# Performance work log

Measured on AMD Instinct MI355X. Metric: run time of the kernel, lower is better.

## Reference

```python
import jax, jax.numpy as jnp
import numpy as np

B, T, E, H = 64, 512, 300, 512


def lstm_scan(x, lens, W, b):
    # x: [B,T,D]; fused LSTM (LSTMBlockFusedCell semantics, forget_bias=1.0,
    # gate order i, j, f, o; outputs zeroed and state held past sequence_length).
    Bx, Tx, _ = x.shape
    Hx = b.shape[0] // 4
    xt = jnp.transpose(x, (1, 0, 2))  # [T,B,D]

    def step(carry, inp):
        c, h = carry
        x_t, t = inp
        z = jnp.concatenate([x_t, h], axis=-1) @ W + b  # [B,4H]
        i, j, f, o = jnp.split(z, 4, axis=-1)
        c_new = jax.nn.sigmoid(f + 1.0) * c + jax.nn.sigmoid(i) * jnp.tanh(j)
        h_new = jax.nn.sigmoid(o) * jnp.tanh(c_new)
        valid = (t < lens)[:, None]
        c2 = jnp.where(valid, c_new, c)
        h2 = jnp.where(valid, h_new, h)
        out = jnp.where(valid, h_new, jnp.zeros_like(h_new))
        return (c2, h2), out

    init = (jnp.zeros((Bx, Hx), x.dtype), jnp.zeros((Bx, Hx), x.dtype))
    _, ys = jax.lax.scan(step, init, (xt, jnp.arange(Tx)))
    return jnp.transpose(ys, (1, 0, 2))  # [B,T,H]


def reverse_seq(x, lens):
    # tf.reverse_sequence along time: reverse first lens[b] steps, keep padding in place
    Tx = x.shape[1]
    t = jnp.arange(Tx)[None, :]
    L = lens[:, None]
    idx = jnp.where(t < L, L - 1 - t, t)  # [B,T]
    return jnp.take_along_axis(x, idx[:, :, None], axis=1)


def bilstm(x, lens, Wf, bf, Wb, bb):
    fw = lstm_scan(x, lens, Wf, bf)
    bw = reverse_seq(lstm_scan(reverse_seq(x, lens), lens, Wb, bb), lens)
    return jnp.concatenate([fw, bw], axis=-1)  # [B,T,2H]


def setup_inputs() -> dict:
    key = jax.random.key(0)
    ks = jax.random.split(key, 8)
    s0 = 1.0 / np.sqrt(E + H)
    s1 = 1.0 / np.sqrt(2 * H + H)
    return {
        "embeddings": jax.random.normal(ks[0], (B, T, E), jnp.float32),
        "nwords": jax.random.randint(ks[1], (B,), 1, T + 1).astype(jnp.int32),
        "W_fw0": jax.random.normal(ks[2], (E + H, 4 * H), jnp.float32) * s0,
        "b_fw0": jnp.zeros((4 * H,), jnp.float32),
        "W_bw0": jax.random.normal(ks[3], (E + H, 4 * H), jnp.float32) * s0,
        "b_bw0": jnp.zeros((4 * H,), jnp.float32),
        "W_fw1": jax.random.normal(ks[4], (2 * H + H, 4 * H), jnp.float32) * s1,
        "b_fw1": jnp.zeros((4 * H,), jnp.float32),
        "W_bw1": jax.random.normal(ks[5], (2 * H + H, 4 * H), jnp.float32) * s1,
        "b_bw1": jnp.zeros((4 * H,), jnp.float32),
    }


def reference(embeddings, nwords, W_fw0, b_fw0, W_bw0, b_bw0,
              W_fw1, b_fw1, W_bw1, b_bw1):
    h = bilstm(embeddings, nwords, W_fw0, b_fw0, W_bw0, b_bw0)  # layer 0
    h = bilstm(h, nwords, W_fw1, b_fw1, W_bw1, b_bw1)           # layer 1
    return h  # [B,T,2H]
```

## Files before the change

### kernel.cpp

```cpp
#include <hip/hip_runtime.h>
#include <hip/hip_bf16.h>


#define Bsz 64
#define Tsz 512
#define Esz 300
#define Hsz 512
#define BT  32768
#define K0P 320
#define K1  1024
#define NG  2048
#define NB  4096

typedef unsigned short ushort_t;
typedef unsigned int   uint_t;
typedef short  short8  __attribute__((ext_vector_type(8)));
typedef float  f32x4   __attribute__((ext_vector_type(4)));

__device__ __forceinline__ f32x4 mfma16(short8 a, short8 b, f32x4 c) {
  return __builtin_amdgcn_mfma_f32_16x16x32_bf16(a, b, c, 0, 0, 0);
}

__device__ __forceinline__ ushort_t f2bf(float f) {
  union { float f; uint_t u; } v; v.f = f;
  uint_t r = v.u + 0x7fffu + ((v.u >> 16) & 1u);
  return (ushort_t)(r >> 16);
}
__device__ __forceinline__ float bf2f(ushort_t s) {
  union { uint_t u; float f; } v; v.u = ((uint_t)s) << 16;
  return v.f;
}
__device__ __forceinline__ float sigm(float x) { return 1.0f / (1.0f + __expf(-x)); }

__global__ void conv_x(const float* __restrict__ x, ushort_t* __restrict__ out) {
  int idx = blockIdx.x * 256 + threadIdx.x;
  int bt = idx / K0P;
  int k  = idx - bt * K0P;
  out[idx] = (k < Esz) ? f2bf(x[(size_t)bt * Esz + k]) : (ushort_t)0;
}

__global__ void transpose_conv(const float* __restrict__ w, int ldw, int krow0,
                               int kvalid, int kpad, ushort_t* __restrict__ out) {
  __shared__ float tile[32][33];
  int kb = blockIdx.x * 32, nb = blockIdx.y * 32;
  int tx = threadIdx.x, ty = threadIdx.y;
#pragma unroll
  for (int tt = 0; tt < 4; ++tt) {
    int k = kb + ty + tt * 8;
    float v = 0.0f;
    if (k < kvalid) v = w[(size_t)(krow0 + k) * ldw + nb + tx];
    tile[ty + tt * 8][tx] = v;
  }
  __syncthreads();
#pragma unroll
  for (int tt = 0; tt < 4; ++tt) {
    int n = nb + ty + tt * 8;
    int k = kb + tx;
    out[(size_t)n * kpad + k] = f2bf(tile[tx][ty + tt * 8]);
  }
}

#define BKg 64
__global__ void __launch_bounds__(256) gemm_bt(
    const ushort_t* __restrict__ A, const ushort_t* __restrict__ Bt,
    const float* __restrict__ bias_fw, const float* __restrict__ bias_bw,
    ushort_t* __restrict__ C, int K) {
  __shared__ __align__(16) ushort_t lA[128 * BKg];
  __shared__ __align__(16) ushort_t lB[128 * BKg];
  int t  = threadIdx.x;
  int m0 = blockIdx.y * 128, n0 = blockIdx.x * 128;
  int w  = t >> 6, l = t & 63;
  int wm = (w >> 1) * 64, wn = (w & 1) * 64;
  int r  = t >> 1, hh = t & 1;
  int lrow = l & 15, lk8 = (l >> 4) * 8;

  f32x4 acc[4][4];
#pragma unroll
  for (int a = 0; a < 4; ++a)
#pragma unroll
    for (int b = 0; b < 4; ++b) acc[a][b] = f32x4{0.f, 0.f, 0.f, 0.f};

  const ushort_t* Ar = A + (size_t)(m0 + r) * K + hh * 32;
  const ushort_t* Br = Bt + (size_t)(n0 + r) * K + hh * 32;

  short8 sa[4], sb[4];
#pragma unroll
  for (int i = 0; i < 4; ++i) {
    sa[i] = *(const short8*)(Ar + i * 8);
    sb[i] = *(const short8*)(Br + i * 8);
  }

  int nk = K / BKg;
  int wr = r * BKg;
  int sw = (r & 7) << 3;
  for (int kb = 0; kb < nk; ++kb) {
    __syncthreads();
#pragma unroll
    for (int i = 0; i < 4; ++i) {
      *(short8*)(lA + wr + ((hh * 32 + i * 8) ^ sw)) = sa[i];
      *(short8*)(lB + wr + ((hh * 32 + i * 8) ^ sw)) = sb[i];
    }
    __syncthreads();
    if (kb + 1 < nk) {
#pragma unroll
      for (int i = 0; i < 4; ++i) {
        sa[i] = *(const short8*)(Ar + (kb + 1) * BKg + i * 8);
        sb[i] = *(const short8*)(Br + (kb + 1) * BKg + i * 8);
      }
    }
#pragma unroll
    for (int kq = 0; kq < 2; ++kq) {
      short8 af[4], bf_[4];
      int kk = kq * 32 + lk8;
#pragma unroll
      for (int ms = 0; ms < 4; ++ms) {
        int row = wm + ms * 16 + lrow;
        af[ms] = *(const short8*)(lA + row * BKg + (kk ^ ((row & 7) << 3)));
      }
#pragma unroll
      for (int ns = 0; ns < 4; ++ns) {
        int row = wn + ns * 16 + lrow;
        bf_[ns] = *(const short8*)(lB + row * BKg + (kk ^ ((row & 7) << 3)));
      }
#pragma unroll
      for (int ms = 0; ms < 4; ++ms)
#pragma unroll
        for (int ns = 0; ns < 4; ++ns)
          acc[ms][ns] = mfma16(af[ms], bf_[ns], acc[ms][ns]);
    }
  }
#pragma unroll
  for (int ns = 0; ns < 4; ++ns) {
    int colg = n0 + wn + ns * 16 + lrow;
    float bv = (colg < NG) ? bias_fw[colg] : bias_bw[colg - NG];
#pragma unroll
    for (int ms = 0; ms < 4; ++ms) {
      int rowg = m0 + wm + ms * 16 + (l >> 4) * 4;
#pragma unroll
      for (int i = 0; i < 4; ++i)
        C[(size_t)(rowg + i) * NB + colg] = f2bf(acc[ms][ns][i] + bv);
    }
  }
}

#define PSLC 32
__global__ void __launch_bounds__(256, 1) lstm_rec(
    const ushort_t* __restrict__ Zx,
    const ushort_t* __restrict__ Wht,
    const int* __restrict__ lens,
    ushort_t* __restrict__ hbuf,
    ushort_t* __restrict__ out16,
    float* __restrict__ out32,
    uint_t* __restrict__ bar)
{
  int t = threadIdx.x;
  int dir = blockIdx.x >> 5, p = blockIdx.x & 31;
  int w = t >> 6, l = t & 63;
  int lrow = l & 15, lq = l >> 4;
  const int dimg = p * 16 + lrow;

  __shared__ __align__(16) ushort_t wl[64 * 512];
  {
    int r = t >> 2, q = t & 3;
    int gcol = (r >> 4) * 512 + p * 16 + (r & 15);
    const ushort_t* src = Wht + ((size_t)dir * NG + gcol) * 512 + q * 128;
    int sw = (r & 7) << 3;
#pragma unroll
    for (int i = 0; i < 16; ++i)
      *(short8*)(wl + r * 512 + ((q * 128 + i * 8) ^ sw)) = *(const short8*)(src + i * 8);
  }
  int lens_r[4];
#pragma unroll
  for (int i = 0; i < 4; ++i) lens_r[i] = lens[w * 16 + lq * 4 + i];
  __syncthreads();

  float    c[4]   = {0.f, 0.f, 0.f, 0.f};
  ushort_t hmy[4] = {0, 0, 0, 0};
  uint_t* mybar = bar + dir * 512;
  int budget = 50000000;

  for (int s = 0; s < Tsz; ++s) {
    const ushort_t* hb = hbuf + ((size_t)(dir * 2 + (s & 1)) * 64) * 512;
    ushort_t*       hw = hbuf + ((size_t)(dir * 2 + ((s & 1) ^ 1)) * 64) * 512;

    int  ttc[4]; bool vld[4]; float zx[4][4];
#pragma unroll
    for (int i = 0; i < 4; ++i) {
      int brow = w * 16 + lq * 4 + i;
      vld[i] = (s < lens_r[i]);
      int tt = dir ? (lens_r[i] - 1 - s) : s;
      if (!vld[i]) tt = 0;
      ttc[i] = tt;
      const ushort_t* zrow = Zx + ((size_t)brow * Tsz + tt) * NB + dir * NG + dimg;
#pragma unroll
      for (int g = 0; g < 4; ++g) zx[i][g] = bf2f(zrow[g * 512]);
    }

    f32x4 acc[4];
#pragma unroll
    for (int g = 0; g < 4; ++g) acc[g] = f32x4{0.f, 0.f, 0.f, 0.f};
#pragma unroll
    for (int kt = 0; kt < 16; ++kt) {
      short8 a = *(const short8*)(hb + (w * 16 + lrow) * 512 + kt * 32 + lq * 8);
#pragma unroll
      for (int g = 0; g < 4; ++g) {
        int row = g * 16 + lrow;
        short8 b = *(const short8*)(wl + row * 512 + ((kt * 32 + lq * 8) ^ ((row & 7) << 3)));
        acc[g] = mfma16(a, b, acc[g]);
      }
    }

#pragma unroll
    for (int i = 0; i < 4; ++i) {
      int brow = w * 16 + lq * 4 + i;
      ushort_t hst = hmy[i];
      if (vld[i]) {
        float z0 = acc[0][i] + zx[i][0];
        float z1 = acc[1][i] + zx[i][1];
        float z2 = acc[2][i] + zx[i][2];
        float z3 = acc[3][i] + zx[i][3];
        float ig = sigm(z0), jg = tanhf(z1), fg = sigm(z2 + 1.0f), og = sigm(z3);
        c[i] = fg * c[i] + ig * jg;
        float hn = og * tanhf(c[i]);
        hst = f2bf(hn);
        hmy[i] = hst;
        size_t oidx = ((size_t)brow * Tsz + ttc[i]) * 1024 + dir * 512 + dimg;
        if (out32) out32[oidx] = hn;
        else       out16[oidx] = hst;
      }
      hw[brow * 512 + dimg] = hst;
    }

    __syncthreads();
    if (t == 0) {
      __builtin_amdgcn_fence(__ATOMIC_RELEASE, "agent");
      atomicAdd(&mybar[s], 1u);
      while (__hip_atomic_load(&mybar[s], __ATOMIC_RELAXED, __HIP_MEMORY_SCOPE_AGENT) < PSLC) {
        __builtin_amdgcn_s_sleep(2);
        if (--budget < 0) break;
      }
      __builtin_amdgcn_fence(__ATOMIC_ACQUIRE, "agent");
    }
    __syncthreads();
  }
}

extern "C" void kernel_launch(void* const* d_in, const int* in_sizes, int n_in,
                              void* d_out, int out_size, void* d_ws, size_t ws_size,
                              hipStream_t stream) {
  (void)in_sizes; (void)n_in; (void)ws_size;
  const float* emb    = (const float*)d_in[0];
  const int*   nwords = (const int*)d_in[1];
  const float* Wf0 = (const float*)d_in[2];
  const float* bf0 = (const float*)d_in[3];
  const float* Wb0 = (const float*)d_in[4];
  const float* bb0 = (const float*)d_in[5];
  const float* Wf1 = (const float*)d_in[6];
  const float* bf1 = (const float*)d_in[7];
  const float* Wb1 = (const float*)d_in[8];
  const float* bb1 = (const float*)d_in[9];

  ushort_t* H0  = (ushort_t*)d_out;
  ushort_t* X16 = (ushort_t*)((char*)d_out + (size_t)BT * 1024 * 2);

  char* ws = (char*)d_ws;
  size_t off = 0;
  auto alloc = [&](size_t bytes) {
    char* pp = ws + off;
    off += (bytes + 255) & ~(size_t)255;
    return pp;
  };
  ushort_t* W0xt = (ushort_t*)alloc((size_t)NB * K0P * 2);
  ushort_t* W0ht = (ushort_t*)alloc((size_t)2 * NG * 512 * 2);
  ushort_t* W1xt = (ushort_t*)alloc((size_t)NB * K1 * 2);
  ushort_t* W1ht = (ushort_t*)alloc((size_t)2 * NG * 512 * 2);
  ushort_t* Zx   = (ushort_t*)alloc((size_t)BT * NB * 2);
  ushort_t* hbuf = (ushort_t*)alloc((size_t)2 * 2 * 64 * 512 * 2);
  uint_t*   bar  = (uint_t*)alloc((size_t)2 * 2 * 512 * 4);

  hipMemsetAsync(d_out, 0, (size_t)out_size * 4, stream);
  hipMemsetAsync(hbuf, 0, (size_t)2 * 2 * 64 * 512 * 2, stream);
  hipMemsetAsync(bar,  0, (size_t)2 * 2 * 512 * 4, stream);

  conv_x<<<dim3(BT * K0P / 256), 256, 0, stream>>>(emb, X16);
  transpose_conv<<<dim3(K0P / 32, 64), dim3(32, 8), 0, stream>>>(Wf0, NG, 0,    Esz,  K0P, W0xt);
  transpose_conv<<<dim3(K0P / 32, 64), dim3(32, 8), 0, stream>>>(Wb0, NG, 0,    Esz,  K0P, W0xt + (size_t)NG * K0P);
  transpose_conv<<<dim3(512 / 32, 64), dim3(32, 8), 0, stream>>>(Wf0, NG, Esz,  512,  512, W0ht);
  transpose_conv<<<dim3(512 / 32, 64), dim3(32, 8), 0, stream>>>(Wb0, NG, Esz,  512,  512, W0ht + (size_t)NG * 512);
  transpose_conv<<<dim3(K1 / 32, 64),  dim3(32, 8), 0, stream>>>(Wf1, NG, 0,    K1,   K1,  W1xt);
  transpose_conv<<<dim3(K1 / 32, 64),  dim3(32, 8), 0, stream>>>(Wb1, NG, 0,    K1,   K1,  W1xt + (size_t)NG * K1);
  transpose_conv<<<dim3(512 / 32, 64), dim3(32, 8), 0, stream>>>(Wf1, NG, K1,   512,  512, W1ht);
  transpose_conv<<<dim3(512 / 32, 64), dim3(32, 8), 0, stream>>>(Wb1, NG, K1,   512,  512, W1ht + (size_t)NG * 512);

  gemm_bt<<<dim3(NB / 128, BT / 128), 256, 0, stream>>>(X16, W0xt, bf0, bb0, Zx, K0P);
  lstm_rec<<<64, 256, 0, stream>>>(Zx, W0ht, nwords, hbuf, H0, nullptr, bar);

  hipMemsetAsync(hbuf, 0, (size_t)2 * 2 * 64 * 512 * 2, stream);

  gemm_bt<<<dim3(NB / 128, BT / 128), 256, 0, stream>>>(H0, W1xt, bf1, bb1, Zx, K1);
  hipMemsetAsync(d_out, 0, (size_t)out_size * 4, stream);
  lstm_rec<<<64, 256, 0, stream>>>(Zx, W1ht, nwords, hbuf, nullptr, (float*)d_out, bar + 1024);
}
```

Baseline: 9.043 ms.

## Replace grid barrier with step-tagged hidden state and per-chunk polling

Removes the per-timestep global atomic barrier in the LSTM recurrence. Each hidden value is now stored as a 32-bit word carrying its bf16 value plus the timestep tag. Consumers poll their own quarter-K chunks until every tag matches, and prefetch the next chunk while computing the current one. The input projection columns are permuted so that each hidden unit's four gates sit next to each other, which lets one 8-byte load fetch all four gates. This trades barrier latency for twice the hidden-buffer traffic and spin polling, and relies on relaxed atomics giving the ordering it needs.

Result: slower. 11.62 ms (+28.5%).

```diff
diff --git a/kernel.cpp b/kernel.cpp
--- a/kernel.cpp
+++ b/kernel.cpp
@@ -14,6 +14,7 @@
 
 typedef unsigned short ushort_t;
 typedef unsigned int   uint_t;
+typedef unsigned long long u64_t;
 typedef short  short8  __attribute__((ext_vector_type(8)));
 typedef float  f32x4   __attribute__((ext_vector_type(4)));
 
@@ -40,7 +41,8 @@
 }
 
 __global__ void transpose_conv(const float* __restrict__ w, int ldw, int krow0,
-                               int kvalid, int kpad, ushort_t* __restrict__ out) {
+                               int kvalid, int kpad, int perm,
+                               ushort_t* __restrict__ out) {
   __shared__ float tile[32][33];
   int kb = blockIdx.x * 32, nb = blockIdx.y * 32;
   int tx = threadIdx.x, ty = threadIdx.y;
@@ -56,7 +58,8 @@
   for (int tt = 0; tt < 4; ++tt) {
     int n = nb + ty + tt * 8;
     int k = kb + tx;
-    out[(size_t)n * kpad + k] = f2bf(tile[tx][ty + tt * 8]);
+    int n2 = perm ? (((n & 511) << 2) | (n >> 9)) : n;
+    out[(size_t)n2 * kpad + k] = f2bf(tile[tx][ty + tt * 8]);
   }
 }
 
@@ -132,7 +135,9 @@
 #pragma unroll
   for (int ns = 0; ns < 4; ++ns) {
     int colg = n0 + wn + ns * 16 + lrow;
-    float bv = (colg < NG) ? bias_fw[colg] : bias_bw[colg - NG];
+    int cp = colg & 2047;
+    int borig = ((cp & 3) << 9) | (cp >> 2);
+    float bv = (colg < NG) ? bias_fw[borig] : bias_bw[borig];
 #pragma unroll
     for (int ms = 0; ms < 4; ++ms) {
       int rowg = m0 + wm + ms * 16 + (l >> 4) * 4;
@@ -143,21 +148,20 @@
   }
 }
 
-#define PSLC 32
 __global__ void __launch_bounds__(256, 1) lstm_rec(
     const ushort_t* __restrict__ Zx,
     const ushort_t* __restrict__ Wht,
     const int* __restrict__ lens,
-    ushort_t* __restrict__ hbuf,
+    uint_t* __restrict__ hbuf32,
     ushort_t* __restrict__ out16,
-    float* __restrict__ out32,
-    uint_t* __restrict__ bar)
+    float* __restrict__ out32)
 {
   int t = threadIdx.x;
   int dir = blockIdx.x >> 5, p = blockIdx.x & 31;
   int w = t >> 6, l = t & 63;
   int lrow = l & 15, lq = l >> 4;
-  const int dimg = p * 16 + lrow;
+  const int dimg  = p * 16 + lrow;
+  const int myrow = w * 16 + lrow;
 
   __shared__ __align__(16) ushort_t wl[64 * 512];
   {
@@ -174,74 +178,116 @@
   for (int i = 0; i < 4; ++i) lens_r[i] = lens[w * 16 + lq * 4 + i];
   __syncthreads();
 
-  float    c[4]   = {0.f, 0.f, 0.f, 0.f};
-  ushort_t hmy[4] = {0, 0, 0, 0};
-  uint_t* mybar = bar + dir * 512;
-  int budget = 50000000;
-
-  for (int s = 0; s < Tsz; ++s) {
-    const ushort_t* hb = hbuf + ((size_t)(dir * 2 + (s & 1)) * 64) * 512;
-    ushort_t*       hw = hbuf + ((size_t)(dir * 2 + ((s & 1) ^ 1)) * 64) * 512;
-
-    int  ttc[4]; bool vld[4]; float zx[4][4];
-#pragma unroll
-    for (int i = 0; i < 4; ++i) {
-      int brow = w * 16 + lq * 4 + i;
-      vld[i] = (s < lens_r[i]);
-      int tt = dir ? (lens_r[i] - 1 - s) : s;
-      if (!vld[i]) tt = 0;
-      ttc[i] = tt;
-      const ushort_t* zrow = Zx + ((size_t)brow * Tsz + tt) * NB + dir * NG + dimg;
-#pragma unroll
-      for (int g = 0; g < 4; ++g) zx[i][g] = bf2f(zrow[g * 512]);
-    }
-
-    f32x4 acc[4];
-#pragma unroll
-    for (int g = 0; g < 4; ++g) acc[g] = f32x4{0.f, 0.f, 0.f, 0.f};
-#pragma unroll
-    for (int kt = 0; kt < 16; ++kt) {
-      short8 a = *(const short8*)(hb + (w * 16 + lrow) * 512 + kt * 32 + lq * 8);
+  uint_t* hb32[2] = {hbuf32 + (size_t)(dir * 2 + 0) * 64 * 512,
+                     hbuf32 + (size_t)(dir * 2 + 1) * 64 * 512};
+  u64_t*  hb64[2] = {(u64_t*)hb32[0], (u64_t*)hb32[1]};
+
+  float  c[4]     = {0.f, 0.f, 0.f, 0.f};
+  uint_t hbits[4] = {0, 0, 0, 0};
+  int    ttc[4], vld[4];
+  uint2  zraw[4];
+  f32x4  acc[4];
+  int budget = 1 << 22;
+
+  const int base64 = myrow * 256 + lq * 4;
+  u64_t bufA[16], bufB[16];
+
+  auto issue = [&](int u, u64_t (&bb)[16]) {
+    if (u >= Tsz * 4) return;
+    int s = u >> 2, q = u & 3;
+    const u64_t* src = hb64[s & 1] + base64 + q * 64;
+#pragma unroll
+    for (int kk = 0; kk < 4; ++kk)
+#pragma unroll
+      for (int m = 0; m < 4; ++m)
+        bb[kk * 4 + m] = __hip_atomic_load(src + kk * 16 + m,
+                          __ATOMIC_RELAXED, __HIP_MEMORY_SCOPE_AGENT);
+  };
+
+  auto unit = [&](int u, u64_t (&cur)[16], u64_t (&nxt)[16]) {
+    int s = u >> 2, q = u & 3;
+    if (q == 0) {
+#pragma unroll
+      for (int i = 0; i < 4; ++i) {
+        int brow = w * 16 + lq * 4 + i;
+        vld[i] = (s < lens_r[i]) ? 1 : 0;
+        int tt = dir ? (lens_r[i] - 1 - s) : s;
+        if (!vld[i]) tt = 0;
+        ttc[i] = tt;
+        zraw[i] = *(const uint2*)(Zx + ((size_t)brow * Tsz + tt) * NB
+                                  + dir * NG + (dimg << 2));
+      }
+#pragma unroll
+      for (int g = 0; g < 4; ++g) acc[g] = f32x4{0.f, 0.f, 0.f, 0.f};
+    }
+    issue(u + 1, nxt);
+
+    const u64_t* src = hb64[s & 1] + base64 + q * 64;
+    uint_t want = (uint_t)s;
+    for (;;) {
+      uint_t bad = 0;
+#pragma unroll
+      for (int m2 = 0; m2 < 16; ++m2) {
+        uint_t lo = (uint_t)cur[m2];
+        uint_t hi = (uint_t)(cur[m2] >> 32);
+        bad |= ((lo ^ want) | (hi ^ want)) & 0xffffu;
+      }
+      if (!bad || --budget < 0) break;
+#pragma unroll
+      for (int kk = 0; kk < 4; ++kk)
+#pragma unroll
+        for (int m = 0; m < 4; ++m)
+          cur[kk * 4 + m] = __hip_atomic_load(src + kk * 16 + m,
+                             __ATOMIC_RELAXED, __HIP_MEMORY_SCOPE_AGENT);
+    }
+
+#pragma unroll
+    for (int kk = 0; kk < 4; ++kk) {
+      int kt = q * 4 + kk;
+      short8 af;
+#pragma unroll
+      for (int m = 0; m < 4; ++m) {
+        af[2 * m]     = (short)((uint_t)cur[kk * 4 + m] >> 16);
+        af[2 * m + 1] = (short)(cur[kk * 4 + m] >> 48);
+      }
 #pragma unroll
       for (int g = 0; g < 4; ++g) {
         int row = g * 16 + lrow;
-        short8 b = *(const short8*)(wl + row * 512 + ((kt * 32 + lq * 8) ^ ((row & 7) << 3)));
-        acc[g] = mfma16(a, b, acc[g]);
-      }
-    }
-
-#pragma unroll
-    for (int i = 0; i < 4; ++i) {
-      int brow = w * 16 + lq * 4 + i;
-      ushort_t hst = hmy[i];
-      if (vld[i]) {
-        float z0 = acc[0][i] + zx[i][0];
-        float z1 = acc[1][i] + zx[i][1];
-        float z2 = acc[2][i] + zx[i][2];
-        float z3 = acc[3][i] + zx[i][3];
-        float ig = sigm(z0), jg = tanhf(z1), fg = sigm(z2 + 1.0f), og = sigm(z3);
-        c[i] = fg * c[i] + ig * jg;
-        float hn = og * tanhf(c[i]);
-        hst = f2bf(hn);
-        hmy[i] = hst;
-        size_t oidx = ((size_t)brow * Tsz + ttc[i]) * 1024 + dir * 512 + dimg;
-        if (out32) out32[oidx] = hn;
-        else       out16[oidx] = hst;
-      }
-      hw[brow * 512 + dimg] = hst;
-    }
-
-    __syncthreads();
-    if (t == 0) {
-      __builtin_amdgcn_fence(__ATOMIC_RELEASE, "agent");
-      atomicAdd(&mybar[s], 1u);
-      while (__hip_atomic_load(&mybar[s], __ATOMIC_RELAXED, __HIP_MEMORY_SCOPE_AGENT) < PSLC) {
-        __builtin_amdgcn_s_sleep(2);
-        if (--budget < 0) break;
-      }
-      __builtin_amdgcn_fence(__ATOMIC_ACQUIRE, "agent");
-    }
-    __syncthreads();
+        short8 bfr = *(const short8*)(wl + row * 512
+                       + ((kt * 32 + lq * 8) ^ ((row & 7) << 3)));
+        acc[g] = mfma16(af, bfr, acc[g]);
+      }
+    }
+
+    if (q == 3) {
+      uint_t* hw = hb32[(s + 1) & 1];
+      uint_t tagn = (uint_t)(s + 1);
+#pragma unroll
+      for (int i = 0; i < 4; ++i) {
+        int brow = w * 16 + lq * 4 + i;
+        if (vld[i]) {
+          float z0 = acc[0][i] + bf2f((ushort_t)(zraw[i].x & 0xffffu));
+          float z1 = acc[1][i] + bf2f((ushort_t)(zraw[i].x >> 16));
+          float z2 = acc[2][i] + bf2f((ushort_t)(zraw[i].y & 0xffffu));
+          float z3 = acc[3][i] + bf2f((ushort_t)(zraw[i].y >> 16));
+          float ig = sigm(z0), jg = tanhf(z1), fg = sigm(z2 + 1.0f), og = sigm(z3);
+          c[i] = fg * c[i] + ig * jg;
+          float hn = og * tanhf(c[i]);
+          hbits[i] = f2bf(hn);
+          size_t oidx = ((size_t)brow * Tsz + ttc[i]) * 1024 + dir * 512 + dimg;
+          if (out32) out32[oidx] = hn;
+          else       out16[oidx] = (ushort_t)hbits[i];
+        }
+        __hip_atomic_store(hw + brow * 512 + dimg, (hbits[i] << 16) | tagn,
+                           __ATOMIC_RELAXED, __HIP_MEMORY_SCOPE_AGENT);
+      }
+    }
+  };
+
+  issue(0, bufA);
+  for (int u = 0; u < Tsz * 4; u += 2) {
+    unit(u,     bufA, bufB);
+    unit(u + 1, bufB, bufA);
   }
 }
 
@@ -275,29 +321,27 @@
   ushort_t* W1xt = (ushort_t*)alloc((size_t)NB * K1 * 2);
   ushort_t* W1ht = (ushort_t*)alloc((size_t)2 * NG * 512 * 2);
   ushort_t* Zx   = (ushort_t*)alloc((size_t)BT * NB * 2);
-  ushort_t* hbuf = (ushort_t*)alloc((size_t)2 * 2 * 64 * 512 * 2);
-  uint_t*   bar  = (uint_t*)alloc((size_t)2 * 2 * 512 * 4);
+  uint_t*   hbuf = (uint_t*)alloc((size_t)2 * 2 * 64 * 512 * 4);
 
   hipMemsetAsync(d_out, 0, (size_t)out_size * 4, stream);
-  hipMemsetAsync(hbuf, 0, (size_t)2 * 2 * 64 * 512 * 2, stream);
-  hipMemsetAsync(bar,  0, (size_t)2 * 2 * 512 * 4, stream);
+  hipMemsetAsync(hbuf, 0, (size_t)2 * 2 * 64 * 512 * 4, stream);
 
   conv_x<<<dim3(BT * K0P / 256), 256, 0, stream>>>(emb, X16);
-  transpose_conv<<<dim3(K0P / 32, 64), dim3(32, 8), 0, stream>>>(Wf0, NG, 0,    Esz,  K0P, W0xt);
-  transpose_conv<<<dim3(K0P / 32, 64), dim3(32, 8), 0, stream>>>(Wb0, NG, 0,    Esz,  K0P, W0xt + (size_t)NG * K0P);
-  transpose_conv<<<dim3(512 / 32, 64), dim3(32, 8), 0, stream>>>(Wf0, NG, Esz,  512,  512, W0ht);
-  transpose_conv<<<dim3(512 / 32, 64), dim3(32, 8), 0, stream>>>(Wb0, NG, Esz,  512,  512, W0ht + (size_t)NG * 512);
-  transpose_conv<<<dim3(K1 / 32, 64),  dim3(32, 8), 0, stream>>>(Wf1, NG, 0,    K1,   K1,  W1xt);
-  transpose_conv<<<dim3(K1 / 32, 64),  dim3(32, 8), 0, stream>>>(Wb1, NG, 0,    K1,   K1,  W1xt + (size_t)NG * K1);
-  transpose_conv<<<dim3(512 / 32, 64), dim3(32, 8), 0, stream>>>(Wf1, NG, K1,   512,  512, W1ht);
-  transpose_conv<<<dim3(512 / 32, 64), dim3(32, 8), 0, stream>>>(Wb1, NG, K1,   512,  512, W1ht + (size_t)NG * 512);
+  transpose_conv<<<dim3(K0P / 32, 64), dim3(32, 8), 0, stream>>>(Wf0, NG, 0,   Esz, K0P, 1, W0xt);
+  transpose_conv<<<dim3(K0P / 32, 64), dim3(32, 8), 0, stream>>>(Wb0, NG, 0,   Esz, K0P, 1, W0xt + (size_t)NG * K0P);
+  transpose_conv<<<dim3(512 / 32, 64), dim3(32, 8), 0, stream>>>(Wf0, NG, Esz, 512, 512, 0, W0ht);
+  transpose_conv<<<dim3(512 / 32, 64), dim3(32, 8), 0, stream>>>(Wb0, NG, Esz, 512, 512, 0, W0ht + (size_t)NG * 512);
+  transpose_conv<<<dim3(K1 / 32, 64),  dim3(32, 8), 0, stream>>>(Wf1, NG, 0,   K1,  K1,  1, W1xt);
+  transpose_conv<<<dim3(K1 / 32, 64),  dim3(32, 8), 0, stream>>>(Wb1, NG, 0,   K1,  K1,  1, W1xt + (size_t)NG * K1);
+  transpose_conv<<<dim3(512 / 32, 64), dim3(32, 8), 0, stream>>>(Wf1, NG, K1,  512, 512, 0, W1ht);
+  transpose_conv<<<dim3(512 / 32, 64), dim3(32, 8), 0, stream>>>(Wb1, NG, K1,  512, 512, 0, W1ht + (size_t)NG * 512);
 
   gemm_bt<<<dim3(NB / 128, BT / 128), 256, 0, stream>>>(X16, W0xt, bf0, bb0, Zx, K0P);
-  lstm_rec<<<64, 256, 0, stream>>>(Zx, W0ht, nwords, hbuf, H0, nullptr, bar);
-
-  hipMemsetAsync(hbuf, 0, (size_t)2 * 2 * 64 * 512 * 2, stream);
+  lstm_rec<<<64, 256, 0, stream>>>(Zx, W0ht, nwords, hbuf, H0, nullptr);
+
+  hipMemsetAsync(hbuf, 0, (size_t)2 * 2 * 64 * 512 * 4, stream);
 
   gemm_bt<<<dim3(NB / 128, BT / 128), 256, 0, stream>>>(H0, W1xt, bf1, bb1, Zx, K1);
   hipMemsetAsync(d_out, 0, (size_t)out_size * 4, stream);
-  lstm_rec<<<64, 256, 0, stream>>>(Zx, W1ht, nwords, hbuf, nullptr, (float*)d_out, bar + 1024);
-}
+  lstm_rec<<<64, 256, 0, stream>>>(Zx, W1ht, nwords, hbuf, nullptr, (float*)d_out);
+}
```
